# Kernel optimization log

Hardware: AMD Instinct MI355X
Metric: run time of the kernel (lower is better)

## Reference

```python
import jax, jax.numpy as jnp
import numpy as np

S, B, E, H, DFF = 1024, 8, 1024, 16, 4096
D = E // H
EPS = 1e-5


def _layernorm(x, g, b):
    m = jnp.mean(x, axis=-1, keepdims=True)
    v = jnp.mean(jnp.square(x - m), axis=-1, keepdims=True)
    return (x - m) * jax.lax.rsqrt(v + EPS) * g + b


def setup_inputs() -> dict:
    key = jax.random.key(0)
    ks = jax.random.split(key, 6)
    return {
        "src": jax.random.normal(ks[0], (S, B, E), jnp.float32),
        "in_proj_w": jax.random.normal(ks[1], (3 * E, E), jnp.float32) * (E ** -0.5),
        "in_proj_b": jnp.zeros((3 * E,), jnp.float32),
        "out_w": jax.random.normal(ks[2], (E, E), jnp.float32) * (E ** -0.5),
        "out_b": jnp.zeros((E,), jnp.float32),
        "ln1_g": jnp.ones((E,), jnp.float32),
        "ln1_b": jnp.zeros((E,), jnp.float32),
        "ln2_g": jnp.ones((E,), jnp.float32),
        "ln2_b": jnp.zeros((E,), jnp.float32),
        "w1": jax.random.normal(ks[3], (DFF, E), jnp.float32) * (E ** -0.5),
        "b1": jnp.zeros((DFF,), jnp.float32),
        "w2": jax.random.normal(ks[4], (E, DFF), jnp.float32) * (DFF ** -0.5),
        "b2": jnp.zeros((E,), jnp.float32),
    }


def reference(src, in_proj_w, in_proj_b, out_w, out_b, ln1_g, ln1_b, ln2_g, ln2_b, w1, b1, w2, b2):
    # src: (S, B, E). Packed in-projection: qkv = src @ W^T + b, split into q,k,v.
    qkv = src @ in_proj_w.T + in_proj_b          # (S, B, 3E)
    q, k, v = jnp.split(qkv, 3, axis=-1)
    q = q.reshape(S, B, H, D)
    k = k.reshape(S, B, H, D)
    v = v.reshape(S, B, H, D)
    # Torch scales q by 1/sqrt(head_dim) before the bmm.
    scores = jnp.einsum("sbhd,tbhd->bhst", q * (D ** -0.5), k)   # (B, H, S, S)
    attn = jax.nn.softmax(scores, axis=-1)
    ctx = jnp.einsum("bhst,tbhd->sbhd", attn, v).reshape(S, B, E)
    attn_out = ctx @ out_w.T + out_b
    # Post-norm encoder layer (norm_first=False), dropout=0.
    x = _layernorm(src + attn_out, ln1_g, ln1_b)
    ff = jax.nn.relu(x @ w1.T + b1) @ w2.T + b2
    return _layernorm(x + ff, ln2_g, ln2_b)
```

## Files before the change

### kernel.cpp

```cpp
#include <hip/hip_runtime.h>

#define S_LEN 1024
#define BATCH 8
#define EMB   1024
#define NH    16
#define HD    64
#define FFD   4096
#define ROWS  (S_LEN*BATCH)

typedef __attribute__((ext_vector_type(8))) short  short8;
typedef __attribute__((ext_vector_type(4))) float  float4v;
typedef __attribute__((ext_vector_type(4))) unsigned int uint4v;

struct alignas(8) us4 { unsigned short x, y, z, w; };

__device__ __forceinline__ unsigned short f2bf(float f) {
    unsigned int u = __float_as_uint(f);
    u += 0x7fffu + ((u >> 16) & 1u);
    return (unsigned short)(u >> 16);
}
__device__ __forceinline__ float bf2f(unsigned short b) {
    return __uint_as_float((unsigned int)b << 16);
}
__device__ __forceinline__ unsigned int cvtpk_bf16(float lo, float hi) {
    unsigned int r;
    asm("v_cvt_pk_bf16_f32 %0, %1, %2" : "=v"(r) : "v"(lo), "v"(hi));
    return r;
}
__device__ __forceinline__ float exp2v(float x) {
    float r;
    asm("v_exp_f32 %0, %1" : "=v"(r) : "v"(x));
    return r;
}

__device__ __forceinline__ void gload_lds16(const void* g, void* l) {
    __builtin_amdgcn_global_load_lds(
        (const __attribute__((address_space(1))) unsigned int*)g,
        (__attribute__((address_space(3))) unsigned int*)l, 16, 0, 0);
}

__device__ __forceinline__ int swz(int row, int chunk) {
    return (row << 7) + ((chunk ^ (row & 7)) << 4);
}

__global__ __launch_bounds__(256) void cast_bf(const float* __restrict__ in,
                                               unsigned short* __restrict__ out,
                                               int n4) {
    int i = blockIdx.x * 256 + threadIdx.x;
    if (i >= n4) return;
    float4 v = ((const float4*)in)[i];
    us4 o = { f2bf(v.x), f2bf(v.y), f2bf(v.z), f2bf(v.w) };
    ((us4*)out)[i] = o;
}

#define QSCALE 0.18033688011112042f
template <int MODE>
__global__ __launch_bounds__(512, 2) void gemm256(const unsigned short* __restrict__ A,
                                                  const unsigned short* __restrict__ Bw,
                                                  const float* __restrict__ bias,
                                                  unsigned short* __restrict__ outb,
                                                  int M, int N, int K) {
    __shared__ char lds[131072];
    const int tid = threadIdx.x, lane = tid & 63, w = tid >> 6;
    const int wr = w >> 2, wc = w & 3;
    const int m0 = blockIdx.y * 256, n0 = blockIdx.x * 256;
    const int nt = K >> 6;

    size_t baseA[2], baseB[2];
    int ldsOff[2];
#pragma unroll
    for (int q = 0; q < 2; ++q) {
        int ci = q * 512 + tid;
        int row = ci >> 3;
        int c = (ci & 7) ^ (row & 7);
        baseA[q] = (size_t)(m0 + row) * K + c * 8;
        baseB[q] = (size_t)(n0 + row) * K + c * 8;
        ldsOff[q] = ci * 16;
    }

    auto stage = [&](int kt, int which) {
        int ktc = kt < nt ? kt : 0;
        int slot = kt & 1;
        if (which < 2) {
#pragma unroll
            for (int q = 0; q < 2; ++q)
                gload_lds16(A + baseA[q] + (size_t)which * 128 * K + (size_t)ktc * 64,
                            lds + slot * 32768 + which * 16384 + ldsOff[q]);
        } else {
            int h = which - 2;
#pragma unroll
            for (int q = 0; q < 2; ++q)
                gload_lds16(Bw + baseB[q] + (size_t)h * 128 * K + (size_t)ktc * 64,
                            lds + 65536 + slot * 32768 + h * 16384 + ldsOff[q]);
        }
    };

    auto rdA = [&](int slot, int mh, int i, int mk) -> short8 {
        int arow = wr * 128 + mh * 64 + i * 16 + (lane & 15);
        return *(const short8*)(lds + slot * 32768 + swz(arow, mk * 4 + (lane >> 4)));
    };
    auto rdB = [&](int slot, int nh, int j, int mk) -> short8 {
        int brow = wc * 64 + nh * 32 + j * 16 + (lane & 15);
        return *(const short8*)(lds + 65536 + slot * 32768 + swz(brow, mk * 4 + (lane >> 4)));
    };

    float4v acc[8][4];
#pragma unroll
    for (int i = 0; i < 8; ++i)
#pragma unroll
        for (int j = 0; j < 4; ++j) acc[i][j] = (float4v){0.f, 0.f, 0.f, 0.f};

    short8 a[4][2], b[2][2][2];

    stage(0, 0); stage(0, 1); stage(0, 2); stage(0, 3);
    stage(1, 0);
    asm volatile("s_waitcnt vmcnt(2)" ::: "memory");
    __builtin_amdgcn_s_barrier();

#define MFMA16(MH, NH)                                                          \
    __builtin_amdgcn_s_setprio(1);                                              \
    _Pragma("unroll")                                                           \
    for (int i = 0; i < 4; ++i)                                                 \
        _Pragma("unroll")                                                       \
        for (int j = 0; j < 2; ++j) {                                           \
            acc[(MH)*4+i][(NH)*2+j] = __builtin_amdgcn_mfma_f32_16x16x32_bf16(  \
                a[i][0], b[NH][j][0], acc[(MH)*4+i][(NH)*2+j], 0, 0, 0);        \
            acc[(MH)*4+i][(NH)*2+j] = __builtin_amdgcn_mfma_f32_16x16x32_bf16(  \
                a[i][1], b[NH][j][1], acc[(MH)*4+i][(NH)*2+j], 0, 0, 0);        \
        }                                                                       \
    __builtin_amdgcn_s_setprio(0);

    for (int t = 0; t < nt; ++t) {
        const int slot = t & 1;
#pragma unroll
        for (int i = 0; i < 4; ++i) {
            a[i][0] = rdA(slot, 0, i, 0);
            a[i][1] = rdA(slot, 0, i, 1);
        }
#pragma unroll
        for (int j = 0; j < 2; ++j) {
            b[0][j][0] = rdB(slot, 0, j, 0);
            b[0][j][1] = rdB(slot, 0, j, 1);
        }
        stage(t + 1, 1);
        __builtin_amdgcn_s_barrier();
        asm volatile("s_waitcnt lgkmcnt(0)" ::: "memory");
        __builtin_amdgcn_sched_barrier(0);
        MFMA16(0, 0)
        __builtin_amdgcn_s_barrier();
#pragma unroll
        for (int j = 0; j < 2; ++j) {
            b[1][j][0] = rdB(slot, 1, j, 0);
            b[1][j][1] = rdB(slot, 1, j, 1);
        }
        stage(t + 1, 2);
        __builtin_amdgcn_s_barrier();
        asm volatile("s_waitcnt lgkmcnt(0)" ::: "memory");
        __builtin_amdgcn_sched_barrier(0);
        MFMA16(0, 1)
        __builtin_amdgcn_s_barrier();
#pragma unroll
        for (int i = 0; i < 4; ++i) {
            a[i][0] = rdA(slot, 1, i, 0);
            a[i][1] = rdA(slot, 1, i, 1);
        }
        stage(t + 1, 3);
        __builtin_amdgcn_s_barrier();
        asm volatile("s_waitcnt lgkmcnt(0)" ::: "memory");
        __builtin_amdgcn_sched_barrier(0);
        MFMA16(1, 1)
        __builtin_amdgcn_s_barrier();
        stage(t + 2, 0);
        MFMA16(1, 0)
        asm volatile("s_waitcnt vmcnt(2)" ::: "memory");
        __builtin_amdgcn_s_barrier();
    }
#undef MFMA16
    asm volatile("s_waitcnt vmcnt(0)" ::: "memory");

#pragma unroll
    for (int mi = 0; mi < 8; ++mi) {
#pragma unroll
        for (int nj = 0; nj < 4; ++nj) {
            int col = n0 + wc * 64 + nj * 16 + (lane & 15);
            float bv = bias[col];
#pragma unroll
            for (int r = 0; r < 4; ++r) {
                int row = m0 + wr * 128 + mi * 16 + (lane >> 4) * 4 + r;
                size_t idx = (size_t)row * N + col;
                float v = acc[mi][nj][r] + bv;
                if (MODE == 0) {
                    if (col < EMB) v *= QSCALE;
                    outb[idx] = f2bf(v);
                } else {
                    outb[idx] = f2bf(fmaxf(v, 0.f));
                }
            }
        }
    }
}

template <int MODE>
__global__ __launch_bounds__(256) void gemm_bt(const unsigned short* __restrict__ A,
                                               const unsigned short* __restrict__ Bw,
                                               const float* __restrict__ bias,
                                               const float* __restrict__ res,
                                               const unsigned short* __restrict__ resb,
                                               float* __restrict__ outf,
                                               int M, int N, int K) {
    __shared__ char As[128 * 64 * 2];
    __shared__ char Bs[128 * 64 * 2];
    const int tid  = threadIdx.x;
    const int lane = tid & 63;
    const int w    = tid >> 6;
    const int wr   = w >> 1, wc = w & 1;
    const int m0 = blockIdx.y * 128, n0 = blockIdx.x * 128;

    size_t aoff[4], boff[4];
#pragma unroll
    for (int p = 0; p < 4; ++p) {
        int ci  = p * 256 + tid;
        int row = ci >> 3;
        int c   = (ci & 7) ^ (row & 7);
        aoff[p] = (size_t)(m0 + row) * K + c * 8;
        boff[p] = (size_t)(n0 + row) * K + c * 8;
    }

    float4v acc[4][4];
#pragma unroll
    for (int i = 0; i < 4; ++i)
#pragma unroll
        for (int j = 0; j < 4; ++j) acc[i][j] = (float4v){0.f, 0.f, 0.f, 0.f};

    for (int k0 = 0; k0 < K; k0 += 64) {
        __syncthreads();
#pragma unroll
        for (int p = 0; p < 4; ++p) {
            gload_lds16(A + aoff[p] + k0, As + (p * 256 + w * 64) * 16);
            gload_lds16(Bw + boff[p] + k0, Bs + (p * 256 + w * 64) * 16);
        }
        __syncthreads();
#pragma unroll
        for (int mk = 0; mk < 2; ++mk) {
            short8 a[4], b[4];
#pragma unroll
            for (int i = 0; i < 4; ++i) {
                int ar = wr * 64 + i * 16 + (lane & 15);
                a[i]   = *(const short8*)(As + swz(ar, mk * 4 + (lane >> 4)));
                int br = wc * 64 + i * 16 + (lane & 15);
                b[i]   = *(const short8*)(Bs + swz(br, mk * 4 + (lane >> 4)));
            }
#pragma unroll
            for (int i = 0; i < 4; ++i)
#pragma unroll
                for (int j = 0; j < 4; ++j)
                    acc[i][j] = __builtin_amdgcn_mfma_f32_16x16x32_bf16(
                        a[i], b[j], acc[i][j], 0, 0, 0);
        }
    }

#pragma unroll
    for (int i = 0; i < 4; ++i) {
#pragma unroll
        for (int j = 0; j < 4; ++j) {
            int col  = n0 + wc * 64 + j * 16 + (lane & 15);
            float bv = bias[col];
#pragma unroll
            for (int r = 0; r < 4; ++r) {
                int row    = m0 + wr * 64 + i * 16 + (lane >> 4) * 4 + r;
                size_t idx = (size_t)row * N + col;
                float v    = acc[i][j][r] + bv;
                if (MODE == 1) outf[idx] = v + res[idx];
                else           outf[idx] = v + bf2f(resb[idx]);
            }
        }
    }
}

__global__ __launch_bounds__(256) void vtrans(const unsigned short* __restrict__ qkv,
                                              unsigned short* __restrict__ vt) {
    const int bh = blockIdx.y, b = bh >> 4, h = bh & 15;
    const int t0 = blockIdx.x * 64;
    const int tid = threadIdx.x;
    __shared__ unsigned short lds[64][72];
#pragma unroll
    for (int rep = 0; rep < 2; ++rep) {
        int slot = rep * 256 + tid;
        int row = slot >> 3, cc = slot & 7;
        const unsigned short* g =
            qkv + ((size_t)(t0 + row) * BATCH + b) * 3072 + 2 * EMB + h * 64 + cc * 8;
        *(uint4v*)&lds[row][cc * 8] = *(const uint4v*)g;
    }
    __syncthreads();
#pragma unroll
    for (int rep = 0; rep < 2; ++rep) {
        int slot = rep * 256 + tid;
        int d = slot >> 3, tc = slot & 7;
        unsigned short tmp[8] __attribute__((aligned(16)));
#pragma unroll
        for (int j = 0; j < 8; ++j) tmp[j] = lds[tc * 8 + j][d];
        unsigned short* g = vt + ((size_t)bh * 64 + d) * S_LEN + t0 + tc * 8;
        *(uint4v*)g = *(const uint4v*)tmp;
    }
}

__global__ __launch_bounds__(256) void attn(const unsigned short* __restrict__ qkv,
                                            const unsigned short* __restrict__ vt,
                                            unsigned short* __restrict__ ctx) {
    __shared__ char Qs[64 * 128];
    __shared__ char Ks[64 * 128];
    __shared__ char Vs[64 * 128];
    __shared__ char Ps[4][16 * 128];
    const int tid = threadIdx.x, lane = tid & 63, w = tid >> 6;
    const int bh = blockIdx.y, b = bh >> 4, h = bh & 15;
    const int s0 = blockIdx.x * 64;
    const int g = lane >> 4, qs = lane & 15;

#pragma unroll
    for (int p = 0; p < 2; ++p) {
        int ci = p * 256 + tid;
        int row = ci >> 3, c = (ci & 7) ^ (row & 7);
        gload_lds16(qkv + ((size_t)(s0 + row) * BATCH + b) * 3072 + h * 64 + c * 8,
                    Qs + (p * 256 + w * 64) * 16);
    }

    float4v O[4];
#pragma unroll
    for (int df = 0; df < 4; ++df) O[df] = (float4v){0.f, 0.f, 0.f, 0.f};
    float m_s = -1e30f;
    float l_s = 0.f;

    for (int t0 = 0; t0 < S_LEN; t0 += 64) {
        __syncthreads();
#pragma unroll
        for (int p = 0; p < 2; ++p) {
            int ci = p * 256 + tid;
            int row = ci >> 3, c = (ci & 7) ^ (row & 7);
            gload_lds16(qkv + ((size_t)(t0 + row) * BATCH + b) * 3072 + EMB + h * 64 + c * 8,
                        Ks + (p * 256 + w * 64) * 16);
            gload_lds16(vt + ((size_t)bh * 64 + row) * S_LEN + t0 + c * 8,
                        Vs + (p * 256 + w * 64) * 16);
        }
        __syncthreads();

        float4v Sf[4];
#pragma unroll
        for (int tf = 0; tf < 4; ++tf) Sf[tf] = (float4v){0.f, 0.f, 0.f, 0.f};
#pragma unroll
        for (int mk = 0; mk < 2; ++mk) {
            int qr = w * 16 + qs;
            short8 qa = *(const short8*)(Qs + swz(qr, mk * 4 + g));
#pragma unroll
            for (int tf = 0; tf < 4; ++tf) {
                int kr = tf * 16 + qs;
                short8 kb = *(const short8*)(Ks + swz(kr, mk * 4 + g));
                Sf[tf] = __builtin_amdgcn_mfma_f32_16x16x32_bf16(kb, qa, Sf[tf], 0, 0, 0);
            }
        }

        float mx = fmaxf(fmaxf(Sf[0][0], Sf[0][1]), fmaxf(Sf[0][2], Sf[0][3]));
#pragma unroll
        for (int tf = 1; tf < 4; ++tf)
            mx = fmaxf(mx, fmaxf(fmaxf(Sf[tf][0], Sf[tf][1]),
                                 fmaxf(Sf[tf][2], Sf[tf][3])));
        mx = fmaxf(mx, __shfl_xor(mx, 16));
        mx = fmaxf(mx, __shfl_xor(mx, 32));

        if (!__all(mx - m_s <= 8.0f)) {
            float mnew = fmaxf(m_s, mx);
            float alpha = exp2v(m_s - mnew);
            m_s = mnew;
            l_s *= alpha;
#pragma unroll
            for (int r = 0; r < 4; ++r) {
                float ar = __shfl(alpha, 4 * g + r);
#pragma unroll
                for (int df = 0; df < 4; ++df) O[df][r] *= ar;
            }
        }

        float rs = 0.f;
#pragma unroll
        for (int tf = 0; tf < 4; ++tf) {
            float p0 = exp2v(Sf[tf][0] - m_s);
            float p1 = exp2v(Sf[tf][1] - m_s);
            float p2 = exp2v(Sf[tf][2] - m_s);
            float p3 = exp2v(Sf[tf][3] - m_s);
            rs += (p0 + p1) + (p2 + p3);
            uint2 pk = make_uint2(cvtpk_bf16(p0, p1), cvtpk_bf16(p2, p3));
            *(uint2*)(Ps[w] + (qs << 7) +
                      (((2 * tf + (g >> 1)) ^ (qs & 7)) << 4) + ((g & 1) << 3)) = pk;
        }
        rs += __shfl_xor(rs, 16);
        rs += __shfl_xor(rs, 32);
        l_s += rs;

        asm volatile("s_waitcnt lgkmcnt(0)" ::: "memory");
        __builtin_amdgcn_sched_barrier(0);

#pragma unroll
        for (int mk = 0; mk < 2; ++mk) {
            short8 pa = *(const short8*)(Ps[w] + swz(qs, mk * 4 + g));
#pragma unroll
            for (int df = 0; df < 4; ++df) {
                int vr = df * 16 + qs;
                short8 vb = *(const short8*)(Vs + swz(vr, mk * 4 + g));
                O[df] = __builtin_amdgcn_mfma_f32_16x16x32_bf16(pa, vb, O[df], 0, 0, 0);
            }
        }
    }

    float inv = __builtin_amdgcn_rcpf(l_s);
#pragma unroll
    for (int r = 0; r < 4; ++r) {
        float ir = __shfl(inv, 4 * g + r);
#pragma unroll
        for (int df = 0; df < 4; ++df) {
            int srow = s0 + w * 16 + g * 4 + r;
            int d    = df * 16 + qs;
            ctx[((size_t)srow * BATCH + b) * EMB + h * 64 + d] = f2bf(O[df][r] * ir);
        }
    }
}

__global__ __launch_bounds__(256) void ln_ker(const float* __restrict__ y,
                                              const float* __restrict__ g,
                                              const float* __restrict__ bta,
                                              float* __restrict__ xo,
                                              unsigned short* __restrict__ xb) {
    const int row = blockIdx.x, tid = threadIdx.x, lane = tid & 63, w = tid >> 6;
    float4 v = ((const float4*)(y + (size_t)row * EMB))[tid];
    float s = v.x + v.y + v.z + v.w;
    float q = v.x * v.x + v.y * v.y + v.z * v.z + v.w * v.w;
#pragma unroll
    for (int m = 1; m < 64; m <<= 1) {
        s += __shfl_xor(s, m);
        q += __shfl_xor(q, m);
    }
    __shared__ float ps[4], pq[4];
    if (lane == 0) { ps[w] = s; pq[w] = q; }
    __syncthreads();
    s = ps[0] + ps[1] + ps[2] + ps[3];
    q = pq[0] + pq[1] + pq[2] + pq[3];
    float mean = s * (1.f / EMB);
    float var  = q * (1.f / EMB) - mean * mean;
    float rstd = rsqrtf(var + 1e-5f);
    float4 gv = ((const float4*)g)[tid];
    float4 bv = ((const float4*)bta)[tid];
    float4 o;
    o.x = (v.x - mean) * rstd * gv.x + bv.x;
    o.y = (v.y - mean) * rstd * gv.y + bv.y;
    o.z = (v.z - mean) * rstd * gv.z + bv.z;
    o.w = (v.w - mean) * rstd * gv.w + bv.w;
    if (xo) ((float4*)(xo + (size_t)row * EMB))[tid] = o;
    if (xb) {
        us4 ob = { f2bf(o.x), f2bf(o.y), f2bf(o.z), f2bf(o.w) };
        ((us4*)(xb + (size_t)row * EMB))[tid] = ob;
    }
}

extern "C" void kernel_launch(void* const* d_in, const int* in_sizes, int n_in,
                              void* d_out, int out_size, void* d_ws, size_t ws_size,
                              hipStream_t stream) {
    (void)in_sizes; (void)n_in; (void)out_size;
    const float* src       = (const float*)d_in[0];
    const float* in_proj_w = (const float*)d_in[1];
    const float* in_proj_b = (const float*)d_in[2];
    const float* out_w     = (const float*)d_in[3];
    const float* out_b     = (const float*)d_in[4];
    const float* ln1_g     = (const float*)d_in[5];
    const float* ln1_b     = (const float*)d_in[6];
    const float* ln2_g     = (const float*)d_in[7];
    const float* ln2_b     = (const float*)d_in[8];
    const float* w1        = (const float*)d_in[9];
    const float* b1        = (const float*)d_in[10];
    const float* w2        = (const float*)d_in[11];
    const float* b2        = (const float*)d_in[12];

    const size_t MB = 1u << 20;
    if (ws_size < 104 * MB) return;

    char* ws = (char*)d_ws;
    unsigned short* wqkvb = (unsigned short*)(ws);
    unsigned short* wob   = (unsigned short*)(ws + 6 * MB);
    unsigned short* w1b   = (unsigned short*)(ws + 8 * MB);
    unsigned short* w2b   = (unsigned short*)(ws + 16 * MB);
    unsigned short* qkvb  = (unsigned short*)(ws + 24 * MB);
    unsigned short* srcbf = (unsigned short*)(ws + 72 * MB);
    unsigned short* vtb   = (unsigned short*)(ws + 88 * MB);
    unsigned short* ctxb  = (unsigned short*)(ws + 72 * MB);
    unsigned short* xbf   = (unsigned short*)(ws + 24 * MB);
    unsigned short* hb    = (unsigned short*)(ws + 40 * MB);
    float*          yout  = (float*)d_out;

    auto castn = [&](const float* in, unsigned short* out, size_t n) {
        int n4 = (int)(n / 4);
        cast_bf<<<(n4 + 255) / 256, 256, 0, stream>>>(in, out, n4);
    };
    castn(src, srcbf, (size_t)ROWS * EMB);
    castn(in_proj_w, wqkvb, (size_t)3 * EMB * EMB);
    castn(out_w, wob, (size_t)EMB * EMB);
    castn(w1, w1b, (size_t)FFD * EMB);
    castn(w2, w2b, (size_t)EMB * FFD);

    gemm256<0><<<dim3(3 * EMB / 256, ROWS / 256), 512, 0, stream>>>(
        srcbf, wqkvb, in_proj_b, qkvb, ROWS, 3 * EMB, EMB);

    vtrans<<<dim3(S_LEN / 64, BATCH * NH), 256, 0, stream>>>(qkvb, vtb);

    attn<<<dim3(S_LEN / 64, BATCH * NH), 256, 0, stream>>>(qkvb, vtb, ctxb);

    gemm_bt<1><<<dim3(EMB / 128, ROWS / 128), 256, 0, stream>>>(
        ctxb, wob, out_b, src, nullptr, yout, ROWS, EMB, EMB);

    ln_ker<<<ROWS, 256, 0, stream>>>(yout, ln1_g, ln1_b, nullptr, xbf);

    gemm256<2><<<dim3(FFD / 256, ROWS / 256), 512, 0, stream>>>(
        xbf, w1b, b1, hb, ROWS, FFD, EMB);

    gemm_bt<3><<<dim3(EMB / 128, ROWS / 128), 256, 0, stream>>>(
        hb, w2b, b2, nullptr, xbf, yout, ROWS, EMB, FFD);

    ln_ker<<<ROWS, 256, 0, stream>>>(yout, ln2_g, ln2_b, (float*)d_out, nullptr);
}
```

Measured before the change: 373.9 us.

## Replace 128x128 residual GEMMs with double-buffered 256x128 pipelined kernel

The out-projection and FFN-down GEMMs move from a simple 128x128 tile kernel with sync-load-sync per K step to a 256x128 tile kernel with 8 waves. The new kernel double-buffers LDS and issues next-tile global-to-LDS loads in three chunks interleaved with MFMA phases, using setprio and explicit waitcnt. The goal is to hide global load latency and raise reuse per block. In exchange it uses 96KB of LDS and more registers, and halves the number of blocks (256 blocks for N=1024), which may leave CUs underused.

```diff
diff --git a/kernel.cpp b/kernel.cpp
--- a/kernel.cpp
+++ b/kernel.cpp
@@ -201,75 +201,150 @@
 }
 
 template <int MODE>
-__global__ __launch_bounds__(256) void gemm_bt(const unsigned short* __restrict__ A,
-                                               const unsigned short* __restrict__ Bw,
-                                               const float* __restrict__ bias,
-                                               const float* __restrict__ res,
-                                               const unsigned short* __restrict__ resb,
-                                               float* __restrict__ outf,
-                                               int M, int N, int K) {
-    __shared__ char As[128 * 64 * 2];
-    __shared__ char Bs[128 * 64 * 2];
-    const int tid  = threadIdx.x;
-    const int lane = tid & 63;
-    const int w    = tid >> 6;
-    const int wr   = w >> 1, wc = w & 1;
-    const int m0 = blockIdx.y * 128, n0 = blockIdx.x * 128;
-
-    size_t aoff[4], boff[4];
-#pragma unroll
-    for (int p = 0; p < 4; ++p) {
-        int ci  = p * 256 + tid;
+__global__ __launch_bounds__(512, 2) void gemm256n(const unsigned short* __restrict__ A,
+                                                   const unsigned short* __restrict__ Bw,
+                                                   const float* __restrict__ bias,
+                                                   const float* __restrict__ res,
+                                                   const unsigned short* __restrict__ resb,
+                                                   float* __restrict__ outf,
+                                                   int M, int N, int K) {
+    __shared__ char lds[98304];
+    const int tid = threadIdx.x, lane = tid & 63, w = tid >> 6;
+    const int wr = w >> 2, wc = w & 3;
+    const int m0 = blockIdx.y * 256, n0 = blockIdx.x * 128;
+    const int nt = K >> 6;
+    const int g = lane >> 4, qs = lane & 15;
+
+    size_t baseA[4], baseB[2];
+    int ldsOffA[4], ldsOffB[2];
+#pragma unroll
+    for (int q = 0; q < 4; ++q) {
+        int ci = q * 512 + tid;
         int row = ci >> 3;
-        int c   = (ci & 7) ^ (row & 7);
-        aoff[p] = (size_t)(m0 + row) * K + c * 8;
-        boff[p] = (size_t)(n0 + row) * K + c * 8;
-    }
-
-    float4v acc[4][4];
-#pragma unroll
-    for (int i = 0; i < 4; ++i)
-#pragma unroll
-        for (int j = 0; j < 4; ++j) acc[i][j] = (float4v){0.f, 0.f, 0.f, 0.f};
-
-    for (int k0 = 0; k0 < K; k0 += 64) {
-        __syncthreads();
-#pragma unroll
-        for (int p = 0; p < 4; ++p) {
-            gload_lds16(A + aoff[p] + k0, As + (p * 256 + w * 64) * 16);
-            gload_lds16(Bw + boff[p] + k0, Bs + (p * 256 + w * 64) * 16);
-        }
-        __syncthreads();
-#pragma unroll
-        for (int mk = 0; mk < 2; ++mk) {
-            short8 a[4], b[4];
-#pragma unroll
-            for (int i = 0; i < 4; ++i) {
-                int ar = wr * 64 + i * 16 + (lane & 15);
-                a[i]   = *(const short8*)(As + swz(ar, mk * 4 + (lane >> 4)));
-                int br = wc * 64 + i * 16 + (lane & 15);
-                b[i]   = *(const short8*)(Bs + swz(br, mk * 4 + (lane >> 4)));
+        int c = (ci & 7) ^ (row & 7);
+        baseA[q] = (size_t)(m0 + row) * K + c * 8;
+        ldsOffA[q] = ci * 16;
+    }
+#pragma unroll
+    for (int q = 0; q < 2; ++q) {
+        int ci = q * 512 + tid;
+        int row = ci >> 3;
+        int c = (ci & 7) ^ (row & 7);
+        baseB[q] = (size_t)(n0 + row) * K + c * 8;
+        ldsOffB[q] = ci * 16;
+    }
+
+    auto stage = [&](int kt, int which) {
+        int ktc = kt < nt ? kt : 0;
+        int slot = kt & 1;
+        if (which < 2) {
+#pragma unroll
+            for (int q = 0; q < 2; ++q) {
+                int qq = which * 2 + q;
+                gload_lds16(A + baseA[qq] + (size_t)ktc * 64,
+                            lds + slot * 32768 + ldsOffA[qq]);
             }
-#pragma unroll
-            for (int i = 0; i < 4; ++i)
-#pragma unroll
-                for (int j = 0; j < 4; ++j)
-                    acc[i][j] = __builtin_amdgcn_mfma_f32_16x16x32_bf16(
-                        a[i], b[j], acc[i][j], 0, 0, 0);
-        }
-    }
-
-#pragma unroll
-    for (int i = 0; i < 4; ++i) {
-#pragma unroll
-        for (int j = 0; j < 4; ++j) {
-            int col  = n0 + wc * 64 + j * 16 + (lane & 15);
+        } else {
+#pragma unroll
+            for (int q = 0; q < 2; ++q)
+                gload_lds16(Bw + baseB[q] + (size_t)ktc * 64,
+                            lds + 65536 + slot * 16384 + ldsOffB[q]);
+        }
+    };
+
+    auto rdA = [&](int slot, int mh, int i, int mk) -> short8 {
+        int arow = wr * 128 + mh * 64 + i * 16 + qs;
+        return *(const short8*)(lds + slot * 32768 + swz(arow, mk * 4 + g));
+    };
+    auto rdB = [&](int slot, int j, int mk) -> short8 {
+        int brow = wc * 32 + j * 16 + qs;
+        return *(const short8*)(lds + 65536 + slot * 16384 + swz(brow, mk * 4 + g));
+    };
+
+    float4v acc[8][2];
+#pragma unroll
+    for (int i = 0; i < 8; ++i)
+#pragma unroll
+        for (int j = 0; j < 2; ++j) acc[i][j] = (float4v){0.f, 0.f, 0.f, 0.f};
+
+    short8 a[4][2], b[2][2];
+
+    stage(0, 0); stage(0, 1); stage(0, 2);
+    stage(1, 0);
+    asm volatile("s_waitcnt vmcnt(2)" ::: "memory");
+    __builtin_amdgcn_s_barrier();
+
+    for (int t = 0; t < nt; ++t) {
+        const int slot = t & 1;
+#pragma unroll
+        for (int i = 0; i < 4; ++i) {
+            a[i][0] = rdA(slot, 0, i, 0);
+            a[i][1] = rdA(slot, 0, i, 1);
+        }
+#pragma unroll
+        for (int j = 0; j < 2; ++j) {
+            b[j][0] = rdB(slot, j, 0);
+            b[j][1] = rdB(slot, j, 1);
+        }
+        stage(t + 1, 1);
+        __builtin_amdgcn_s_barrier();
+        asm volatile("s_waitcnt lgkmcnt(0)" ::: "memory");
+        __builtin_amdgcn_sched_barrier(0);
+        __builtin_amdgcn_s_setprio(1);
+#pragma unroll
+        for (int i = 0; i < 4; ++i)
+#pragma unroll
+            for (int j = 0; j < 2; ++j) {
+                acc[i][j] = __builtin_amdgcn_mfma_f32_16x16x32_bf16(
+                    a[i][0], b[j][0], acc[i][j], 0, 0, 0);
+                acc[i][j] = __builtin_amdgcn_mfma_f32_16x16x32_bf16(
+                    a[i][1], b[j][1], acc[i][j], 0, 0, 0);
+            }
+        __builtin_amdgcn_s_setprio(0);
+        __builtin_amdgcn_s_barrier();
+#pragma unroll
+        for (int i = 0; i < 4; ++i) {
+            a[i][0] = rdA(slot, 1, i, 0);
+            a[i][1] = rdA(slot, 1, i, 1);
+        }
+        stage(t + 1, 2);
+        __builtin_amdgcn_s_barrier();
+        asm volatile("s_waitcnt lgkmcnt(0)" ::: "memory");
+        __builtin_amdgcn_sched_barrier(0);
+        __builtin_amdgcn_s_setprio(1);
+#pragma unroll
+        for (int i = 0; i < 4; ++i)
+#pragma unroll
+            for (int j = 0; j < 2; ++j)
+                acc[4 + i][j] = __builtin_amdgcn_mfma_f32_16x16x32_bf16(
+                    a[i][0], b[j][0], acc[4 + i][j], 0, 0, 0);
+        __builtin_amdgcn_s_setprio(0);
+        __builtin_amdgcn_s_barrier();
+        stage(t + 2, 0);
+        __builtin_amdgcn_s_setprio(1);
+#pragma unroll
+        for (int i = 0; i < 4; ++i)
+#pragma unroll
+            for (int j = 0; j < 2; ++j)
+                acc[4 + i][j] = __builtin_amdgcn_mfma_f32_16x16x32_bf16(
+                    a[i][1], b[j][1], acc[4 + i][j], 0, 0, 0);
+        __builtin_amdgcn_s_setprio(0);
+        asm volatile("s_waitcnt vmcnt(2)" ::: "memory");
+        __builtin_amdgcn_s_barrier();
+    }
+    asm volatile("s_waitcnt vmcnt(0)" ::: "memory");
+
+#pragma unroll
+    for (int mi = 0; mi < 8; ++mi) {
+#pragma unroll
+        for (int j = 0; j < 2; ++j) {
+            int col = n0 + wc * 32 + j * 16 + qs;
             float bv = bias[col];
 #pragma unroll
             for (int r = 0; r < 4; ++r) {
-                int row    = m0 + wr * 64 + i * 16 + (lane >> 4) * 4 + r;
+                int row = m0 + wr * 128 + mi * 16 + g * 4 + r;
                 size_t idx = (size_t)row * N + col;
-                float v    = acc[i][j][r] + bv;
+                float v = acc[mi][j][r] + bv;
                 if (MODE == 1) outf[idx] = v + res[idx];
                 else           outf[idx] = v + bf2f(resb[idx]);
             }
@@ -510,7 +585,7 @@
 
     attn<<<dim3(S_LEN / 64, BATCH * NH), 256, 0, stream>>>(qkvb, vtb, ctxb);
 
-    gemm_bt<1><<<dim3(EMB / 128, ROWS / 128), 256, 0, stream>>>(
+    gemm256n<1><<<dim3(EMB / 128, ROWS / 256), 512, 0, stream>>>(
         ctxb, wob, out_b, src, nullptr, yout, ROWS, EMB, EMB);
 
     ln_ker<<<ROWS, 256, 0, stream>>>(yout, ln1_g, ln1_b, nullptr, xbf);
@@ -518,7 +593,7 @@
     gemm256<2><<<dim3(FFD / 256, ROWS / 256), 512, 0, stream>>>(
         xbf, w1b, b1, hb, ROWS, FFD, EMB);
 
-    gemm_bt<3><<<dim3(EMB / 128, ROWS / 128), 256, 0, stream>>>(
+    gemm256n<3><<<dim3(EMB / 128, ROWS / 256), 512, 0, stream>>>(
         hb, w2b, b2, nullptr, xbf, yout, ROWS, EMB, FFD);
 
     ln_ker<<<ROWS, 256, 0, stream>>>(yout, ln2_g, ln2_b, (float*)d_out, nullptr);
```

Result: no change. 379.7 us (+1.5%).

## Replace 128-tile output GEMMs with split-K 256-tile GEMM and XCD-aware block mapping

Applied to the files above, without the earlier changes.

Drops the simple 128x128 gemm_bt kernel. The out-projection and FFN2 GEMMs now run on the pipelined 256x256 gemm256 kernel with split-K by two: one half writes fp32 plus bias and residual, the other writes a bf16 partial that the layernorm kernel adds back in. Launch grids become 1D with a remapping that groups M-tiles by blockIdx modulo 8, which looks aimed at L2 locality across XCDs. The workspace is reshuffled so buffers can be aliased. The bf16 partial sum loses some precision, and the extra partial traffic is a cost.

```diff
diff --git a/kernel.cpp b/kernel.cpp
--- a/kernel.cpp
+++ b/kernel.cpp
@@ -58,13 +58,24 @@
 __global__ __launch_bounds__(512, 2) void gemm256(const unsigned short* __restrict__ A,
                                                   const unsigned short* __restrict__ Bw,
                                                   const float* __restrict__ bias,
+                                                  const float* __restrict__ res,
+                                                  const unsigned short* __restrict__ resb,
+                                                  float* __restrict__ outf,
                                                   unsigned short* __restrict__ outb,
-                                                  int M, int N, int K) {
+                                                  unsigned short* __restrict__ outp,
+                                                  int M, int N, int Kc, int ldk) {
     __shared__ char lds[131072];
     const int tid = threadIdx.x, lane = tid & 63, w = tid >> 6;
     const int wr = w >> 2, wc = w & 3;
-    const int m0 = blockIdx.y * 256, n0 = blockIdx.x * 256;
-    const int nt = K >> 6;
+    const int k = blockIdx.x & 7, j = blockIdx.x >> 3;
+    const int ly = k * 4 + (j & 3);
+    int lx, kz;
+    if (MODE >= 4) { lx = (j >> 2) & 3; kz = j >> 4; }
+    else           { lx = j >> 2;       kz = 0; }
+    const int m0 = ly * 256, n0 = lx * 256;
+    const int nt = Kc >> 6;
+    const unsigned short* Ae = A  + (size_t)kz * Kc;
+    const unsigned short* Be = Bw + (size_t)kz * Kc;
 
     size_t baseA[2], baseB[2];
     int ldsOff[2];
@@ -73,8 +84,8 @@
         int ci = q * 512 + tid;
         int row = ci >> 3;
         int c = (ci & 7) ^ (row & 7);
-        baseA[q] = (size_t)(m0 + row) * K + c * 8;
-        baseB[q] = (size_t)(n0 + row) * K + c * 8;
+        baseA[q] = (size_t)(m0 + row) * ldk + c * 8;
+        baseB[q] = (size_t)(n0 + row) * ldk + c * 8;
         ldsOff[q] = ci * 16;
     }
 
@@ -84,13 +95,13 @@
         if (which < 2) {
 #pragma unroll
             for (int q = 0; q < 2; ++q)
-                gload_lds16(A + baseA[q] + (size_t)which * 128 * K + (size_t)ktc * 64,
+                gload_lds16(Ae + baseA[q] + (size_t)which * 128 * ldk + (size_t)ktc * 64,
                             lds + slot * 32768 + which * 16384 + ldsOff[q]);
         } else {
             int h = which - 2;
 #pragma unroll
             for (int q = 0; q < 2; ++q)
-                gload_lds16(Bw + baseB[q] + (size_t)h * 128 * K + (size_t)ktc * 64,
+                gload_lds16(Be + baseB[q] + (size_t)h * 128 * ldk + (size_t)ktc * 64,
                             lds + 65536 + slot * 32768 + h * 16384 + ldsOff[q]);
         }
     };
@@ -99,8 +110,8 @@
         int arow = wr * 128 + mh * 64 + i * 16 + (lane & 15);
         return *(const short8*)(lds + slot * 32768 + swz(arow, mk * 4 + (lane >> 4)));
     };
-    auto rdB = [&](int slot, int nh, int j, int mk) -> short8 {
-        int brow = wc * 64 + nh * 32 + j * 16 + (lane & 15);
+    auto rdB = [&](int slot, int nh, int jj, int mk) -> short8 {
+        int brow = wc * 64 + nh * 32 + jj * 16 + (lane & 15);
         return *(const short8*)(lds + 65536 + slot * 32768 + swz(brow, mk * 4 + (lane >> 4)));
     };
 
@@ -108,7 +119,7 @@
 #pragma unroll
     for (int i = 0; i < 8; ++i)
 #pragma unroll
-        for (int j = 0; j < 4; ++j) acc[i][j] = (float4v){0.f, 0.f, 0.f, 0.f};
+        for (int jj = 0; jj < 4; ++jj) acc[i][jj] = (float4v){0.f, 0.f, 0.f, 0.f};
 
     short8 a[4][2], b[2][2][2];
 
@@ -122,11 +133,11 @@
     _Pragma("unroll")                                                           \
     for (int i = 0; i < 4; ++i)                                                 \
         _Pragma("unroll")                                                       \
-        for (int j = 0; j < 2; ++j) {                                           \
-            acc[(MH)*4+i][(NH)*2+j] = __builtin_amdgcn_mfma_f32_16x16x32_bf16(  \
-                a[i][0], b[NH][j][0], acc[(MH)*4+i][(NH)*2+j], 0, 0, 0);        \
-            acc[(MH)*4+i][(NH)*2+j] = __builtin_amdgcn_mfma_f32_16x16x32_bf16(  \
-                a[i][1], b[NH][j][1], acc[(MH)*4+i][(NH)*2+j], 0, 0, 0);        \
+        for (int jj = 0; jj < 2; ++jj) {                                        \
+            acc[(MH)*4+i][(NH)*2+jj] = __builtin_amdgcn_mfma_f32_16x16x32_bf16( \
+                a[i][0], b[NH][jj][0], acc[(MH)*4+i][(NH)*2+jj], 0, 0, 0);      \
+            acc[(MH)*4+i][(NH)*2+jj] = __builtin_amdgcn_mfma_f32_16x16x32_bf16( \
+                a[i][1], b[NH][jj][1], acc[(MH)*4+i][(NH)*2+jj], 0, 0, 0);      \
         }                                                                       \
     __builtin_amdgcn_s_setprio(0);
 
@@ -138,9 +149,9 @@
             a[i][1] = rdA(slot, 0, i, 1);
         }
 #pragma unroll
-        for (int j = 0; j < 2; ++j) {
-            b[0][j][0] = rdB(slot, 0, j, 0);
-            b[0][j][1] = rdB(slot, 0, j, 1);
+        for (int jj = 0; jj < 2; ++jj) {
+            b[0][jj][0] = rdB(slot, 0, jj, 0);
+            b[0][jj][1] = rdB(slot, 0, jj, 1);
         }
         stage(t + 1, 1);
         __builtin_amdgcn_s_barrier();
@@ -149,9 +160,9 @@
         MFMA16(0, 0)
         __builtin_amdgcn_s_barrier();
 #pragma unroll
-        for (int j = 0; j < 2; ++j) {
-            b[1][j][0] = rdB(slot, 1, j, 0);
-            b[1][j][1] = rdB(slot, 1, j, 1);
+        for (int jj = 0; jj < 2; ++jj) {
+            b[1][jj][0] = rdB(slot, 1, jj, 0);
+            b[1][jj][1] = rdB(slot, 1, jj, 1);
         }
         stage(t + 1, 2);
         __builtin_amdgcn_s_barrier();
@@ -183,7 +194,7 @@
 #pragma unroll
         for (int nj = 0; nj < 4; ++nj) {
             int col = n0 + wc * 64 + nj * 16 + (lane & 15);
-            float bv = bias[col];
+            float bv = (MODE >= 4 && kz == 1) ? 0.f : bias[col];
 #pragma unroll
             for (int r = 0; r < 4; ++r) {
                 int row = m0 + wr * 128 + mi * 16 + (lane >> 4) * 4 + r;
@@ -192,86 +203,16 @@
                 if (MODE == 0) {
                     if (col < EMB) v *= QSCALE;
                     outb[idx] = f2bf(v);
+                } else if (MODE == 2) {
+                    outb[idx] = f2bf(fmaxf(v, 0.f));
                 } else {
-                    outb[idx] = f2bf(fmaxf(v, 0.f));
+                    if (kz == 0) {
+                        float rr = (MODE == 4) ? res[idx] : bf2f(resb[idx]);
+                        outf[idx] = v + rr;
+                    } else {
+                        outp[idx] = f2bf(v);
+                    }
                 }
-            }
-        }
-    }
-}
-
-template <int MODE>
-__global__ __launch_bounds__(256) void gemm_bt(const unsigned short* __restrict__ A,
-                                               const unsigned short* __restrict__ Bw,
-                                               const float* __restrict__ bias,
-                                               const float* __restrict__ res,
-                                               const unsigned short* __restrict__ resb,
-                                               float* __restrict__ outf,
-                                               int M, int N, int K) {
-    __shared__ char As[128 * 64 * 2];
-    __shared__ char Bs[128 * 64 * 2];
-    const int tid  = threadIdx.x;
-    const int lane = tid & 63;
-    const int w    = tid >> 6;
-    const int wr   = w >> 1, wc = w & 1;
-    const int m0 = blockIdx.y * 128, n0 = blockIdx.x * 128;
-
-    size_t aoff[4], boff[4];
-#pragma unroll
-    for (int p = 0; p < 4; ++p) {
-        int ci  = p * 256 + tid;
-        int row = ci >> 3;
-        int c   = (ci & 7) ^ (row & 7);
-        aoff[p] = (size_t)(m0 + row) * K + c * 8;
-        boff[p] = (size_t)(n0 + row) * K + c * 8;
-    }
-
-    float4v acc[4][4];
-#pragma unroll
-    for (int i = 0; i < 4; ++i)
-#pragma unroll
-        for (int j = 0; j < 4; ++j) acc[i][j] = (float4v){0.f, 0.f, 0.f, 0.f};
-
-    for (int k0 = 0; k0 < K; k0 += 64) {
-        __syncthreads();
-#pragma unroll
-        for (int p = 0; p < 4; ++p) {
-            gload_lds16(A + aoff[p] + k0, As + (p * 256 + w * 64) * 16);
-            gload_lds16(Bw + boff[p] + k0, Bs + (p * 256 + w * 64) * 16);
-        }
-        __syncthreads();
-#pragma unroll
-        for (int mk = 0; mk < 2; ++mk) {
-            short8 a[4], b[4];
-#pragma unroll
-            for (int i = 0; i < 4; ++i) {
-                int ar = wr * 64 + i * 16 + (lane & 15);
-                a[i]   = *(const short8*)(As + swz(ar, mk * 4 + (lane >> 4)));
-                int br = wc * 64 + i * 16 + (lane & 15);
-                b[i]   = *(const short8*)(Bs + swz(br, mk * 4 + (lane >> 4)));
-            }
-#pragma unroll
-            for (int i = 0; i < 4; ++i)
-#pragma unroll
-                for (int j = 0; j < 4; ++j)
-                    acc[i][j] = __builtin_amdgcn_mfma_f32_16x16x32_bf16(
-                        a[i], b[j], acc[i][j], 0, 0, 0);
-        }
-    }
-
-#pragma unroll
-    for (int i = 0; i < 4; ++i) {
-#pragma unroll
-        for (int j = 0; j < 4; ++j) {
-            int col  = n0 + wc * 64 + j * 16 + (lane & 15);
-            float bv = bias[col];
-#pragma unroll
-            for (int r = 0; r < 4; ++r) {
-                int row    = m0 + wr * 64 + i * 16 + (lane >> 4) * 4 + r;
-                size_t idx = (size_t)row * N + col;
-                float v    = acc[i][j][r] + bv;
-                if (MODE == 1) outf[idx] = v + res[idx];
-                else           outf[idx] = v + bf2f(resb[idx]);
             }
         }
     }
@@ -298,7 +239,7 @@
         int d = slot >> 3, tc = slot & 7;
         unsigned short tmp[8] __attribute__((aligned(16)));
 #pragma unroll
-        for (int j = 0; j < 8; ++j) tmp[j] = lds[tc * 8 + j][d];
+        for (int jj = 0; jj < 8; ++jj) tmp[jj] = lds[tc * 8 + jj][d];
         unsigned short* g = vt + ((size_t)bh * 64 + d) * S_LEN + t0 + tc * 8;
         *(uint4v*)g = *(const uint4v*)tmp;
     }
@@ -312,8 +253,8 @@
     __shared__ char Vs[64 * 128];
     __shared__ char Ps[4][16 * 128];
     const int tid = threadIdx.x, lane = tid & 63, w = tid >> 6;
-    const int bh = blockIdx.y, b = bh >> 4, h = bh & 15;
-    const int s0 = blockIdx.x * 64;
+    const int bh = blockIdx.x & 127, b = bh >> 4, h = bh & 15;
+    const int s0 = (blockIdx.x >> 7) * 64;
     const int g = lane >> 4, qs = lane & 15;
 
 #pragma unroll
@@ -424,12 +365,17 @@
 }
 
 __global__ __launch_bounds__(256) void ln_ker(const float* __restrict__ y,
+                                              const unsigned short* __restrict__ p1,
                                               const float* __restrict__ g,
                                               const float* __restrict__ bta,
                                               float* __restrict__ xo,
                                               unsigned short* __restrict__ xb) {
     const int row = blockIdx.x, tid = threadIdx.x, lane = tid & 63, w = tid >> 6;
     float4 v = ((const float4*)(y + (size_t)row * EMB))[tid];
+    if (p1) {
+        us4 pv = ((const us4*)(p1 + (size_t)row * EMB))[tid];
+        v.x += bf2f(pv.x); v.y += bf2f(pv.y); v.z += bf2f(pv.z); v.w += bf2f(pv.w);
+    }
     float s = v.x + v.y + v.z + v.w;
     float q = v.x * v.x + v.y * v.y + v.z * v.z + v.w * v.w;
 #pragma unroll
@@ -481,16 +427,17 @@
     if (ws_size < 104 * MB) return;
 
     char* ws = (char*)d_ws;
-    unsigned short* wqkvb = (unsigned short*)(ws);
-    unsigned short* wob   = (unsigned short*)(ws + 6 * MB);
-    unsigned short* w1b   = (unsigned short*)(ws + 8 * MB);
-    unsigned short* w2b   = (unsigned short*)(ws + 16 * MB);
-    unsigned short* qkvb  = (unsigned short*)(ws + 24 * MB);
-    unsigned short* srcbf = (unsigned short*)(ws + 72 * MB);
-    unsigned short* vtb   = (unsigned short*)(ws + 88 * MB);
-    unsigned short* ctxb  = (unsigned short*)(ws + 72 * MB);
-    unsigned short* xbf   = (unsigned short*)(ws + 24 * MB);
-    unsigned short* hb    = (unsigned short*)(ws + 40 * MB);
+    unsigned short* w2b   = (unsigned short*)(ws);
+    unsigned short* ctxb  = (unsigned short*)(ws + 8 * MB);
+    unsigned short* xbf   = (unsigned short*)(ws + 8 * MB);
+    unsigned short* wqkvb = (unsigned short*)(ws + 24 * MB);
+    unsigned short* wob   = (unsigned short*)(ws + 30 * MB);
+    unsigned short* qkvb  = (unsigned short*)(ws + 32 * MB);
+    unsigned short* hb    = (unsigned short*)(ws + 24 * MB);
+    unsigned short* vtb   = (unsigned short*)(ws + 80 * MB);
+    unsigned short* srcbf = (unsigned short*)(ws + 88 * MB);
+    unsigned short* p1    = (unsigned short*)(ws + 88 * MB);
+    unsigned short* w1b   = (unsigned short*)(ws + 88 * MB);
     float*          yout  = (float*)d_out;
 
     auto castn = [&](const float* in, unsigned short* out, size_t n) {
@@ -500,26 +447,31 @@
     castn(src, srcbf, (size_t)ROWS * EMB);
     castn(in_proj_w, wqkvb, (size_t)3 * EMB * EMB);
     castn(out_w, wob, (size_t)EMB * EMB);
+    castn(w2, w2b, (size_t)EMB * FFD);
+
+    gemm256<0><<<(3 * EMB / 256) * 32, 512, 0, stream>>>(
+        srcbf, wqkvb, in_proj_b, nullptr, nullptr,
+        nullptr, qkvb, nullptr, ROWS, 3 * EMB, EMB, EMB);
+
+    vtrans<<<dim3(S_LEN / 64, BATCH * NH), 256, 0, stream>>>(qkvb, vtb);
+
+    attn<<<(S_LEN / 64) * BATCH * NH, 256, 0, stream>>>(qkvb, vtb, ctxb);
+
+    gemm256<4><<<256, 512, 0, stream>>>(
+        ctxb, wob, out_b, src, nullptr,
+        yout, nullptr, p1, ROWS, EMB, EMB / 2, EMB);
+
+    ln_ker<<<ROWS, 256, 0, stream>>>(yout, p1, ln1_g, ln1_b, nullptr, xbf);
+
     castn(w1, w1b, (size_t)FFD * EMB);
-    castn(w2, w2b, (size_t)EMB * FFD);
-
-    gemm256<0><<<dim3(3 * EMB / 256, ROWS / 256), 512, 0, stream>>>(
-        srcbf, wqkvb, in_proj_b, qkvb, ROWS, 3 * EMB, EMB);
-
-    vtrans<<<dim3(S_LEN / 64, BATCH * NH), 256, 0, stream>>>(qkvb, vtb);
-
-    attn<<<dim3(S_LEN / 64, BATCH * NH), 256, 0, stream>>>(qkvb, vtb, ctxb);
-
-    gemm_bt<1><<<dim3(EMB / 128, ROWS / 128), 256, 0, stream>>>(
-        ctxb, wob, out_b, src, nullptr, yout, ROWS, EMB, EMB);
-
-    ln_ker<<<ROWS, 256, 0, stream>>>(yout, ln1_g, ln1_b, nullptr, xbf);
-
-    gemm256<2><<<dim3(FFD / 256, ROWS / 256), 512, 0, stream>>>(
-        xbf, w1b, b1, hb, ROWS, FFD, EMB);
-
-    gemm_bt<3><<<dim3(EMB / 128, ROWS / 128), 256, 0, stream>>>(
-        hb, w2b, b2, nullptr, xbf, yout, ROWS, EMB, FFD);
-
-    ln_ker<<<ROWS, 256, 0, stream>>>(yout, ln2_g, ln2_b, (float*)d_out, nullptr);
-}
+
+    gemm256<2><<<(FFD / 256) * 32, 512, 0, stream>>>(
+        xbf, w1b, b1, nullptr, nullptr,
+        nullptr, hb, nullptr, ROWS, FFD, EMB, EMB);
+
+    gemm256<5><<<256, 512, 0, stream>>>(
+        hb, w2b, b2, nullptr, xbf,
+        yout, nullptr, p1, ROWS, EMB, FFD / 2, FFD);
+
+    ln_ker<<<ROWS, 256, 0, stream>>>(yout, p1, ln2_g, ln2_b, (float*)d_out, nullptr);
+}
```

Result: slower. 396.9 us (+6.1%).
